# Kernel optimization log

Measured on AMD Instinct MI355X. Metric: run time of the kernel, lower is better.

Reference implementation:

```python
import jax, jax.numpy as jnp
import numpy as np

NUM_NODES = 100000
NODE_FEAT_DIM = 512
EDGE_FEAT_DIM = 512
MEM_DIM = NODE_FEAT_DIM + EDGE_FEAT_DIM  # 1024
BATCH = 65536


def setup_inputs() -> dict:
    key = jax.random.key(0)
    k_ids, k_mem, k_emb, kq, ks, kk = jax.random.split(key, 6)
    scale = 1.0 / np.sqrt(MEM_DIM)
    inp = {
        "node_ids": jax.random.randint(k_ids, (BATCH,), 0, NUM_NODES, dtype=jnp.int64)
        if jax.config.jax_enable_x64 else
        jax.random.randint(k_ids, (BATCH,), 0, NUM_NODES, dtype=jnp.int32),
        # memory bank: (N, 1, D); randomized (instead of the zero init) so math is non-trivial
        "node_memories": jax.random.normal(k_mem, (NUM_NODES, 1, MEM_DIM), dtype=jnp.float32) * 0.02,
        "node_embedding": jax.random.normal(k_emb, (NUM_NODES, MEM_DIM), dtype=jnp.float32) * 0.02,
        "Wq": jax.random.normal(jax.random.fold_in(kq, 0), (MEM_DIM, NODE_FEAT_DIM), dtype=jnp.float32) * scale,
        "bq": jnp.zeros((NODE_FEAT_DIM,), dtype=jnp.float32),
        "Ws": jax.random.normal(jax.random.fold_in(ks, 0), (MEM_DIM, NODE_FEAT_DIM), dtype=jnp.float32) * scale,
        "bs": jnp.zeros((NODE_FEAT_DIM,), dtype=jnp.float32),
        "Wk": jax.random.normal(jax.random.fold_in(kk, 0), (MEM_DIM, NODE_FEAT_DIM), dtype=jnp.float32) * scale,
        "bk": jnp.zeros((NODE_FEAT_DIM,), dtype=jnp.float32),
    }
    return inp


def reference(node_ids, node_memories, node_embedding, Wq, bq, Ws, bs, Wk, bk):
    ids = node_ids.astype(jnp.int32)
    # torch.sum(node_memories[ids], dim=2): reduces feature dim -> (B, 1)
    mem_sum = jnp.sum(node_memories[ids], axis=2)          # (B, 1)
    x = mem_sum + node_embedding[ids]                      # broadcast -> (B, D)
    q = jax.nn.sigmoid(x @ Wq + bq)                        # (B, node_feat_dim)
    s = jax.nn.sigmoid(x @ Ws + bs)
    k = jax.nn.sigmoid(x @ Wk + bk)
    return (q, s, k)
```

## Files before the change

### kernel.cpp

```cpp
#include <hip/hip_runtime.h>
#include <hip/hip_bf16.h>
#include <stdint.h>

#define BATCH_N 65536
#define KDIM 1024
#define NTOT 1536

typedef __bf16 bf16x8 __attribute__((ext_vector_type(8)));
typedef float f32x4 __attribute__((ext_vector_type(4)));

__device__ __forceinline__ unsigned short f2bf(float f) {
    unsigned u = __builtin_bit_cast(unsigned, f);
    u += 0x7FFFu + ((u >> 16) & 1u);
    return (unsigned short)(u >> 16);
}

__global__ __launch_bounds__(256) void prep_kernel(
    const int* __restrict__ ids,
    const float* __restrict__ mem,
    const float* __restrict__ emb,
    unsigned short* __restrict__ x)
{
    const int b    = blockIdx.x * 4 + (threadIdx.x >> 6);
    const int lane = threadIdx.x & 63;
    const int id   = ids[b];
    const float4* m4 = (const float4*)(mem + (size_t)id * KDIM) + lane;
    const float4* e4 = (const float4*)(emb + (size_t)id * KDIM) + lane;
    float4 v0 = m4[0];
    float4 v1 = m4[64];
    float4 v2 = m4[128];
    float4 v3 = m4[192];
    float s = (v0.x + v0.y + v0.z + v0.w) + (v1.x + v1.y + v1.z + v1.w)
            + (v2.x + v2.y + v2.z + v2.w) + (v3.x + v3.y + v3.z + v3.w);
    #pragma unroll
    for (int off = 1; off < 64; off <<= 1) s += __shfl_xor(s, off, 64);
    unsigned short* xb = x + (size_t)b * KDIM;
    #pragma unroll
    for (int q = 0; q < 4; ++q) {
        float4 e = e4[q * 64];
        ushort4 o;
        o.x = f2bf(s + e.x);
        o.y = f2bf(s + e.y);
        o.z = f2bf(s + e.z);
        o.w = f2bf(s + e.w);
        const int k   = q * 256 + lane * 4;
        const int ksw = k ^ ((b & 7) << 3);
        *(ushort4*)(xb + ksw) = o;
    }
}

__global__ __launch_bounds__(256) void wconv_kernel(
    const float* __restrict__ Wq, const float* __restrict__ Ws,
    const float* __restrict__ Wk, unsigned short* __restrict__ wt)
{
    const int gt = blockIdx.x * 256 + threadIdx.x;
    const int n  = gt % NTOT;
    const int kb = (gt / NTOT) * 4;
    const float* W = (n < 512) ? Wq : ((n < 1024) ? Ws : Wk);
    const int nn = n & 511;
    ushort4 o;
    o.x = f2bf(W[(size_t)(kb + 0) * 512 + nn]);
    o.y = f2bf(W[(size_t)(kb + 1) * 512 + nn]);
    o.z = f2bf(W[(size_t)(kb + 2) * 512 + nn]);
    o.w = f2bf(W[(size_t)(kb + 3) * 512 + nn]);
    const int ksw = kb ^ ((n & 7) << 3);
    *(ushort4*)(wt + (size_t)n * KDIM + ksw) = o;
}

#define BM 256
#define BN 256
#define BK 64
#define MT (BATCH_N / BM)
#define NT (NTOT / BN)
#define NWG (MT * NT)

#define BAR() asm volatile("s_barrier" ::: "memory")
#define VM6() asm volatile("s_waitcnt vmcnt(6)" ::: "memory")
#define VM0() asm volatile("s_waitcnt vmcnt(0)" ::: "memory")
#define AS1 __attribute__((address_space(1)))
#define AS3 __attribute__((address_space(3)))

__global__ __launch_bounds__(512, 2) void gemm_kernel(
    const unsigned short* __restrict__ X,
    const unsigned short* __restrict__ Wt,
    const float* __restrict__ bq, const float* __restrict__ bs,
    const float* __restrict__ bk, float* __restrict__ out)
{
    __shared__ __align__(16) unsigned short sA[32768];
    __shared__ __align__(16) unsigned short sB[32768];

    const int tid  = threadIdx.x;
    const int xcd  = blockIdx.x & 7;
    const int idx  = blockIdx.x >> 3;
    const int wgid = xcd * (NWG / 8) + idx;
    const int nt   = wgid % NT;
    const int mt   = wgid / NT;
    const int m0   = mt * BM;
    const int n0   = nt * BN;
    const int wid  = tid >> 6;
    const int lane = tid & 63;
    const int wm   = wid >> 2;
    const int wn   = wid & 3;
    const int r16  = lane & 15;
    const int kb0  = (lane >> 4) << 4;
    const int ksw  = (r16 & 7) << 4;

    f32x4 acc[8][4];
    #pragma unroll
    for (int i = 0; i < 8; i++)
        #pragma unroll
        for (int j = 0; j < 4; j++)
            acc[i][j] = f32x4{0.f, 0.f, 0.f, 0.f};

    bf16x8 af0[4][2], af1[4][2], bfr0[2][2], bfr1[2][2];

    const unsigned short* gA = X  + (size_t)(m0 + (tid >> 3)) * KDIM + (tid & 7) * 8;
    const unsigned short* gB = Wt + (size_t)(n0 + (tid >> 3)) * KDIM + (tid & 7) * 8;
    const int ldst = (tid & 448) * 8;

#define STG_A(slot, h, kt) do {                                                 \
    _Pragma("unroll")                                                            \
    for (int c = 0; c < 2; ++c)                                                  \
        __builtin_amdgcn_global_load_lds(                                        \
            (const AS1 void*)(gA + (size_t)((h) * 128 + c * 64) * KDIM + (kt) * BK), \
            (AS3 void*)(&sA[((slot) * 2 + (h)) * 8192 + c * 4096 + ldst]),       \
            16, 0, 0);                                                           \
} while (0)
#define STG_B(slot, h, kt) do {                                                 \
    _Pragma("unroll")                                                            \
    for (int c = 0; c < 2; ++c)                                                  \
        __builtin_amdgcn_global_load_lds(                                        \
            (const AS1 void*)(gB + (size_t)((h) * 128 + c * 64) * KDIM + (kt) * BK), \
            (AS3 void*)(&sB[((slot) * 2 + (h)) * 8192 + c * 4096 + ldst]),       \
            16, 0, 0);                                                           \
} while (0)

#define LDA(SET, slot, qa) do {                                                 \
    const char* p = (const char*)&sA[((slot) * 2 + (qa)) * 8192];                \
    _Pragma("unroll")                                                            \
    for (int i = 0; i < 4; ++i)                                                  \
        _Pragma("unroll")                                                        \
        for (int kk = 0; kk < 2; ++kk)                                           \
            SET[i][kk] = *(const bf16x8*)(p + (wm * 64 + i * 16 + r16) * 128     \
                                            + ((kk * 64 + kb0) ^ ksw));          \
} while (0)
#define LDB(SET, slot, qb) do {                                                 \
    const char* p = (const char*)&sB[((slot) * 2 + (qb)) * 8192];                \
    _Pragma("unroll")                                                            \
    for (int j = 0; j < 2; ++j)                                                  \
        _Pragma("unroll")                                                        \
        for (int kk = 0; kk < 2; ++kk)                                           \
            SET[j][kk] = *(const bf16x8*)(p + (wn * 32 + j * 16 + r16) * 128     \
                                            + ((kk * 64 + kb0) ^ ksw));          \
} while (0)

#define MM(QA, QB, ASET, BSET) do {                                             \
    __builtin_amdgcn_s_setprio(1);                                               \
    _Pragma("unroll")                                                            \
    for (int i = 0; i < 4; ++i)                                                  \
        _Pragma("unroll")                                                        \
        for (int j = 0; j < 2; ++j)                                              \
            _Pragma("unroll")                                                    \
            for (int kk = 0; kk < 2; ++kk)                                       \
                acc[(QA) * 4 + i][(QB) * 2 + j] =                                \
                    __builtin_amdgcn_mfma_f32_16x16x32_bf16(                     \
                        ASET[i][kk], BSET[j][kk],                                \
                        acc[(QA) * 4 + i][(QB) * 2 + j], 0, 0, 0);               \
    __builtin_amdgcn_s_setprio(0);                                               \
} while (0)

    STG_A(0, 0, 0); STG_A(0, 1, 0); STG_B(0, 0, 0); STG_B(0, 1, 0);
    STG_A(1, 0, 1); STG_B(1, 1, 1); STG_A(1, 1, 1);
    VM0();
    BAR();

    #pragma unroll 1
    for (int t = 0; t < 7; ++t) {
        const int ka = 2 * t + 1, kb2 = 2 * t + 2, kc = 2 * t + 3;
        LDA(af0, 0, 0); LDB(bfr0, 0, 0);
        MM(0, 0, af0, bfr0);
        LDB(bfr1, 0, 1); STG_B(1, 0, ka);                        BAR();
        MM(0, 1, af0, bfr1);
        LDA(af1, 0, 1); STG_A(0, 0, kb2);                        BAR();
        MM(1, 1, af1, bfr1); STG_B(0, 1, kb2);                   BAR();
        MM(1, 0, af1, bfr0); STG_A(0, 1, kb2); VM6();            BAR();
        LDA(af0, 1, 0); LDB(bfr0, 1, 0);
        MM(0, 0, af0, bfr0);
        LDB(bfr1, 1, 1); STG_B(0, 0, kb2);                       BAR();
        MM(0, 1, af0, bfr1);
        LDA(af1, 1, 1); STG_A(1, 0, kc);                         BAR();
        MM(1, 1, af1, bfr1); STG_B(1, 1, kc);                    BAR();
        MM(1, 0, af1, bfr0); STG_A(1, 1, kc); VM6();             BAR();
    }
    LDA(af0, 0, 0); LDB(bfr0, 0, 0);
    MM(0, 0, af0, bfr0);
    LDB(bfr1, 0, 1); STG_B(1, 0, 15);                            BAR();
    MM(0, 1, af0, bfr1); LDA(af1, 0, 1);                         BAR();
    MM(1, 1, af1, bfr1);                                         BAR();
    MM(1, 0, af1, bfr0); VM0();                                  BAR();
    LDA(af0, 1, 0); LDB(bfr0, 1, 0);
    MM(0, 0, af0, bfr0);
    LDB(bfr1, 1, 1);                                             BAR();
    MM(0, 1, af0, bfr1); LDA(af1, 1, 1);                         BAR();
    MM(1, 1, af1, bfr1);                                         BAR();
    MM(1, 0, af1, bfr0);

    const int grp = nt >> 1;
    const float* bias = (grp == 0) ? bq : ((grp == 1) ? bs : bk);
    float* obase = out + (size_t)grp * ((size_t)BATCH_N * 512);
    const int cb = (nt & 1) * 256;
    #pragma unroll
    for (int qb = 0; qb < 2; ++qb)
        #pragma unroll
        for (int j = 0; j < 2; ++j) {
            const int col = cb + qb * 128 + wn * 32 + j * 16 + r16;
            const float bv = bias[col];
            #pragma unroll
            for (int qa = 0; qa < 2; ++qa)
                #pragma unroll
                for (int i = 0; i < 4; ++i) {
                    const int rbase = m0 + qa * 128 + wm * 64 + i * 16 + ((lane >> 4) << 2);
                    #pragma unroll
                    for (int r = 0; r < 4; ++r) {
                        float v = acc[qa * 4 + i][qb * 2 + j][r] + bv;
                        v = 1.0f / (1.0f + __expf(-v));
                        __builtin_nontemporal_store(v, &obase[(size_t)(rbase + r) * 512 + col]);
                    }
                }
        }
#undef STG_A
#undef STG_B
#undef LDA
#undef LDB
#undef MM
}

extern "C" void kernel_launch(void* const* d_in, const int* in_sizes, int n_in,
                              void* d_out, int out_size, void* d_ws, size_t ws_size,
                              hipStream_t stream) {
    const int*   ids = (const int*)d_in[0];
    const float* mem = (const float*)d_in[1];
    const float* emb = (const float*)d_in[2];
    const float* Wq  = (const float*)d_in[3];
    const float* bq  = (const float*)d_in[4];
    const float* Ws  = (const float*)d_in[5];
    const float* bs  = (const float*)d_in[6];
    const float* Wk  = (const float*)d_in[7];
    const float* bk  = (const float*)d_in[8];
    float* out = (float*)d_out;

    unsigned short* x  = (unsigned short*)d_ws;
    unsigned short* wt = x + (size_t)BATCH_N * KDIM;

    hipLaunchKernelGGL(wconv_kernel, dim3(NTOT), dim3(256), 0, stream, Wq, Ws, Wk, wt);
    hipLaunchKernelGGL(prep_kernel, dim3(BATCH_N / 4), dim3(256), 0, stream, ids, mem, emb, x);
    hipLaunchKernelGGL(gemm_kernel, dim3(NWG), dim3(512), 0, stream,
                       x, wt, bq, bs, bk, out);
}
```

Measured before the change: 391.3 us.

## Replace interleaved 8-barrier GEMM pipeline with simple double-buffered tile loop

Replaces the finely interleaved main loop of the bf16 MFMA GEMM with a plain double-buffered scheme. Each tile now issues all global-to-LDS stages for the next K tile up front, loads all fragments, runs the four MFMA quadrants, then waits on vmcnt(0) and takes one barrier. The old schedule used a partial vmcnt(6) wait and a barrier after every quadrant. The intent is to cut barrier and wait overhead and simplify the schedule, at the cost of less fine-grained overlap between global loads, LDS reads and MFMA work.

```diff
diff --git a/kernel.cpp b/kernel.cpp
--- a/kernel.cpp
+++ b/kernel.cpp
@@ -75,7 +75,6 @@
 #define NWG (MT * NT)
 
 #define BAR() asm volatile("s_barrier" ::: "memory")
-#define VM6() asm volatile("s_waitcnt vmcnt(6)" ::: "memory")
 #define VM0() asm volatile("s_waitcnt vmcnt(0)" ::: "memory")
 #define AS1 __attribute__((address_space(1)))
 #define AS3 __attribute__((address_space(3)))
@@ -169,41 +168,29 @@
     __builtin_amdgcn_s_setprio(0);                                               \
 } while (0)
 
+#define TILE(S, NS, KTN, DOSTAGE) do {                                          \
+    if (DOSTAGE) {                                                               \
+        STG_A(NS, 0, KTN); STG_A(NS, 1, KTN);                                    \
+        STG_B(NS, 0, KTN); STG_B(NS, 1, KTN);                                    \
+    }                                                                            \
+    LDA(af0, S, 0); LDB(bfr0, S, 0);                                             \
+    LDA(af1, S, 1); LDB(bfr1, S, 1);                                             \
+    MM(0, 0, af0, bfr0); MM(0, 1, af0, bfr1);                                    \
+    MM(1, 1, af1, bfr1); MM(1, 0, af1, bfr0);                                    \
+    VM0(); BAR();                                                                \
+} while (0)
+
     STG_A(0, 0, 0); STG_A(0, 1, 0); STG_B(0, 0, 0); STG_B(0, 1, 0);
-    STG_A(1, 0, 1); STG_B(1, 1, 1); STG_A(1, 1, 1);
     VM0();
     BAR();
 
     #pragma unroll 1
     for (int t = 0; t < 7; ++t) {
-        const int ka = 2 * t + 1, kb2 = 2 * t + 2, kc = 2 * t + 3;
-        LDA(af0, 0, 0); LDB(bfr0, 0, 0);
-        MM(0, 0, af0, bfr0);
-        LDB(bfr1, 0, 1); STG_B(1, 0, ka);                        BAR();
-        MM(0, 1, af0, bfr1);
-        LDA(af1, 0, 1); STG_A(0, 0, kb2);                        BAR();
-        MM(1, 1, af1, bfr1); STG_B(0, 1, kb2);                   BAR();
-        MM(1, 0, af1, bfr0); STG_A(0, 1, kb2); VM6();            BAR();
-        LDA(af0, 1, 0); LDB(bfr0, 1, 0);
-        MM(0, 0, af0, bfr0);
-        LDB(bfr1, 1, 1); STG_B(0, 0, kb2);                       BAR();
-        MM(0, 1, af0, bfr1);
-        LDA(af1, 1, 1); STG_A(1, 0, kc);                         BAR();
-        MM(1, 1, af1, bfr1); STG_B(1, 1, kc);                    BAR();
-        MM(1, 0, af1, bfr0); STG_A(1, 1, kc); VM6();             BAR();
+        TILE(0, 1, 2 * t + 1, 1);
+        TILE(1, 0, 2 * t + 2, 1);
     }
-    LDA(af0, 0, 0); LDB(bfr0, 0, 0);
-    MM(0, 0, af0, bfr0);
-    LDB(bfr1, 0, 1); STG_B(1, 0, 15);                            BAR();
-    MM(0, 1, af0, bfr1); LDA(af1, 0, 1);                         BAR();
-    MM(1, 1, af1, bfr1);                                         BAR();
-    MM(1, 0, af1, bfr0); VM0();                                  BAR();
-    LDA(af0, 1, 0); LDB(bfr0, 1, 0);
-    MM(0, 0, af0, bfr0);
-    LDB(bfr1, 1, 1);                                             BAR();
-    MM(0, 1, af0, bfr1); LDA(af1, 1, 1);                         BAR();
-    MM(1, 1, af1, bfr1);                                         BAR();
-    MM(1, 0, af1, bfr0);
+    TILE(0, 1, 15, 1);
+    TILE(1, 0, 0, 0);
 
     const int grp = nt >> 1;
     const float* bias = (grp == 0) ? bq : ((grp == 1) ? bs : bk);
@@ -233,6 +220,7 @@
 #undef LDA
 #undef LDB
 #undef MM
+#undef TILE
 }
 
 extern "C" void kernel_launch(void* const* d_in, const int* in_sizes, int n_in,
```

After: 432.6 us. 10.6% more time.
